# Kernel tuning notes

Measured on AMD Instinct MI355X. Metric: run time of the kernel, lower is better.

The kernel has to match this reference:

```python
import jax, jax.numpy as jnp
import numpy as np

IN_DIM, H1, H2, N_CLS, N_DOM = 7, 64, 128, 9, 2
N_S, E_S = 100000, 3200000
N_C, E_C = 512, 16384


def gcn_conv(x, edge_index, W, b):
    # PyG GCNConv: x' = D^{-1/2} (A + I) D^{-1/2} (x W) + b
    N = x.shape[0]
    h = x @ W
    loops = jnp.arange(N)
    row = jnp.concatenate([edge_index[0], loops])  # sources
    col = jnp.concatenate([edge_index[1], loops])  # targets
    deg = jax.ops.segment_sum(jnp.ones_like(col, dtype=h.dtype), col, num_segments=N)
    dis = jnp.where(deg > 0, jax.lax.rsqrt(deg), 0.0)
    norm = dis[row] * dis[col]
    out = jax.ops.segment_sum(h[row] * norm[:, None], col, num_segments=N)
    return out + b


def setup_inputs() -> dict:
    key = jax.random.key(0)
    ks = jax.random.split(key, 24)
    d = {}
    d['x_s'] = jax.random.normal(ks[0], (N_S, IN_DIM), dtype=jnp.float32)
    d['x_c'] = jax.random.normal(ks[1], (N_C, IN_DIM), dtype=jnp.float32)
    d['Q'] = jax.random.uniform(ks[2], (N_S, N_C), dtype=jnp.float32)
    d['edge_index_s'] = jax.random.randint(ks[3], (2, E_S), 0, N_S)
    d['edge_index_c'] = jax.random.randint(ks[4], (2, E_C), 0, N_C)
    s = 0.1
    d['W1s'] = jax.random.normal(ks[5], (IN_DIM, H1)) * s
    d['b1s'] = jnp.zeros((H1,), jnp.float32)
    d['W2s'] = jax.random.normal(ks[6], (H1, H2)) * s
    d['b2s'] = jnp.zeros((H2,), jnp.float32)
    d['W1c'] = jax.random.normal(ks[7], (IN_DIM, H1)) * s
    d['b1c'] = jnp.zeros((H1,), jnp.float32)
    d['W2c'] = jax.random.normal(ks[8], (H1, H2)) * s
    d['b2c'] = jnp.zeros((H2,), jnp.float32)
    d['A1'] = jax.random.normal(ks[9], (2 * H2, H2)) * s
    d['ab1'] = jnp.zeros((H2,), jnp.float32)
    d['A2'] = jax.random.normal(ks[10], (H2, 2)) * s
    d['ab2'] = jnp.zeros((2,), jnp.float32)
    d['Wcls'] = jax.random.normal(ks[11], (H2, N_CLS)) * s
    d['bcls'] = jnp.zeros((N_CLS,), jnp.float32)
    d['D1'] = jax.random.normal(ks[12], (H2, H1)) * s
    d['db1'] = jnp.zeros((H1,), jnp.float32)
    d['D2'] = jax.random.normal(ks[13], (H1, N_DOM)) * s
    d['db2'] = jnp.zeros((N_DOM,), jnp.float32)
    return d


def reference(x_s, x_c, Q, edge_index_s, edge_index_c,
              W1s, b1s, W2s, b2s, W1c, b1c, W2c, b2c,
              A1, ab1, A2, ab2, Wcls, bcls, D1, db1, D2, db2):
    # sample branch (eval mode: dropout is identity)
    xs = jax.nn.relu(gcn_conv(x_s, edge_index_s, W1s, b1s))
    xs = jax.nn.relu(gcn_conv(xs, edge_index_s, W2s, b2s))
    # cluster branch
    xc = jax.nn.relu(gcn_conv(x_c, edge_index_c, W1c, b1c))
    xc = jax.nn.relu(gcn_conv(xc, edge_index_c, W2c, b2c))
    # cross-graph decode
    xc_dec = Q @ xc  # [N_s, 128]
    fusion = jnp.concatenate([xs, xc_dec], axis=1)  # [N_s, 256]
    w = jax.nn.softmax(jax.nn.relu(fusion @ A1 + ab1) @ A2 + ab2, axis=1)
    fused = w[:, 0:1] * xs + w[:, 1:2] * xc_dec
    class_output = fused @ Wcls + bcls
    # gradient reversal is identity in forward
    domain_output = jax.nn.relu(fused @ D1 + db1) @ D2 + db2
    return (class_output, domain_output, fused)
```

## Files before the change

kernel.cpp:

```cpp
#include <hip/hip_runtime.h>
#include <cstdint>
#include <cstddef>

static constexpr int kNS = 100000;
static constexpr int kNC = 512;
static constexpr int kES = 3200000;
static constexpr int kEC = 16384;

static constexpr int kNB = (kNS + 63) / 64;
static constexpr int kNB8 = kNB * 8;
static constexpr int kCHUNK = 8192;
static constexpr int kNBLK = (kES + kCHUNK - 1) / kCHUNK;

static constexpr int kGemmQBlocks = (kNS + 63) / 64;
static constexpr int kAgg64Blocks = (kNS + 7) / 8;

typedef __attribute__((ext_vector_type(8))) short short8;
typedef __attribute__((ext_vector_type(4))) float f32x4;

__device__ __forceinline__ unsigned short f2bf(float f) {
  union { float f; unsigned u; } v; v.f = f;
  unsigned u = v.u;
  unsigned r = (u + 0x7fffu + ((u >> 16) & 1u)) >> 16;
  return (unsigned short)r;
}
__device__ __forceinline__ float bflo(unsigned v) { return __uint_as_float(v << 16); }
__device__ __forceinline__ float bfhi(unsigned v) { return __uint_as_float(v & 0xffff0000u); }
__device__ __forceinline__ float bf2f(unsigned short s) { return __uint_as_float(((unsigned)s) << 16); }

__global__ __launch_bounds__(256) void k_passA(const int* __restrict__ col, int E,
                                               int* __restrict__ counts) {
  __shared__ int hist[kNB];
  int t = threadIdx.x, bid = blockIdx.x;
  for (int j = t; j < kNB; j += 256) hist[j] = 0;
  __syncthreads();
  int base = bid * kCHUNK;
#pragma unroll 4
  for (int i = 0; i < kCHUNK / 256; i++) {
    int e = base + i * 256 + t;
    if (e < E) atomicAdd(&hist[col[e] >> 6], 1);
  }
  __syncthreads();
  int sub = bid & 7;
  for (int j = t; j < kNB; j += 256) {
    int v = hist[j];
    if (v) atomicAdd(&counts[j * 8 + sub], v);
  }
}

__global__ void k_scan_flat(const int* __restrict__ cnt, int n, int* __restrict__ starts,
                            int* __restrict__ cursor) {
  __shared__ int s[256];
  int t = threadIdx.x;
  int run = 0;
  for (int base = 0; base < n; base += 256) {
    int i = base + t;
    int v = (i < n) ? cnt[i] : 0;
    s[t] = v;
    __syncthreads();
    for (int o = 1; o < 256; o <<= 1) {
      int x = (t >= o) ? s[t - o] : 0;
      __syncthreads();
      s[t] += x;
      __syncthreads();
    }
    if (i < n) {
      int ex = run + s[t] - v;
      starts[i] = ex;
      cursor[i] = ex;
    }
    int tot = s[255];
    __syncthreads();
    run += tot;
  }
  if (t == 0) starts[n] = run;
}

__global__ __launch_bounds__(256) void k_passB(const int* __restrict__ row, const int* __restrict__ col,
                                               int E, int* __restrict__ cursor, unsigned* __restrict__ edg) {
  __shared__ int hist[kNB];
  int t = threadIdx.x, bid = blockIdx.x;
  int sub = bid & 7;
  for (int j = t; j < kNB; j += 256) hist[j] = 0;
  __syncthreads();
  int base = bid * kCHUNK;
#pragma unroll 4
  for (int i = 0; i < kCHUNK / 256; i++) {
    int e = base + i * 256 + t;
    if (e < E) atomicAdd(&hist[col[e] >> 6], 1);
  }
  __syncthreads();
  for (int j = t; j < kNB; j += 256) {
    int v = hist[j];
    hist[j] = v ? atomicAdd(&cursor[j * 8 + sub], v) : 0;
  }
  __syncthreads();
#pragma unroll 4
  for (int i = 0; i < kCHUNK / 256; i++) {
    int e = base + i * 256 + t;
    if (e < E) {
      int c = col[e];
      int pos = atomicAdd(&hist[c >> 6], 1);
      edg[pos] = ((unsigned)row[e] << 6) | (unsigned)(c & 63);
    }
  }
}

__global__ __launch_bounds__(256) void k_passC(const unsigned* __restrict__ edg,
                                               const int* __restrict__ bstarts,
                                               int* __restrict__ deg, int* __restrict__ nstarts,
                                               float* __restrict__ dis,
                                               int* __restrict__ srow, int N) {
  __shared__ int ldeg[64];
  __shared__ int lcur[64];
  int b = blockIdx.x, t = threadIdx.x;
  int s0 = bstarts[b * 8], s1 = bstarts[b * 8 + 8];
  if (t < 64) ldeg[t] = 0;
  __syncthreads();
  for (int i = s0 + t; i < s1; i += 256) atomicAdd(&ldeg[edg[i] & 63u], 1);
  __syncthreads();
  if (t < 64) {
    int own = ldeg[t];
    int incl = own;
#pragma unroll
    for (int off = 1; off < 64; off <<= 1) {
      int o = __shfl_up(incl, off);
      if (t >= off) incl += o;
    }
    int st = s0 + incl - own;
    lcur[t] = st;
    int g = b * 64 + t;
    if (g < N) {
      deg[g] = own;
      nstarts[g] = st;
      dis[g] = rsqrtf((float)(own + 1));
    }
  }
  __syncthreads();
  for (int i = s0 + t; i < s1; i += 256) {
    unsigned ew = edg[i];
    int pos = atomicAdd(&lcur[ew & 63u], 1);
    srow[pos] = (int)(ew >> 6);
  }
}

__global__ void k_hist(const int* __restrict__ col, int E, int* __restrict__ cnt) {
  int i = blockIdx.x * blockDim.x + threadIdx.x;
  if (i < E) atomicAdd(&cnt[col[i]], 1);
}

__global__ void k_dis(const int* __restrict__ cnt, int N, float* __restrict__ dis) {
  int i = blockIdx.x * blockDim.x + threadIdx.x;
  if (i < N) dis[i] = rsqrtf((float)(cnt[i] + 1));
}

__global__ void k_scan1(const int* __restrict__ cnt, int N, int* __restrict__ starts, int* __restrict__ bsum) {
  __shared__ int s[256];
  int t = threadIdx.x;
  int i = blockIdx.x * 256 + t;
  int v = (i < N) ? cnt[i] : 0;
  s[t] = v;
  __syncthreads();
  for (int o = 1; o < 256; o <<= 1) {
    int x = (t >= o) ? s[t - o] : 0;
    __syncthreads();
    s[t] += x;
    __syncthreads();
  }
  if (i < N) starts[i] = s[t] - v;
  if (t == 255) bsum[blockIdx.x] = s[255];
}

__global__ void k_scan2(int* __restrict__ bsum, int nb) {
  __shared__ int s[256];
  int t = threadIdx.x;
  int run = 0;
  for (int base = 0; base < nb; base += 256) {
    int i = base + t;
    int v = (i < nb) ? bsum[i] : 0;
    s[t] = v;
    __syncthreads();
    for (int o = 1; o < 256; o <<= 1) {
      int x = (t >= o) ? s[t - o] : 0;
      __syncthreads();
      s[t] += x;
      __syncthreads();
    }
    if (i < nb) bsum[i] = run + s[t] - v;
    int tot = s[255];
    __syncthreads();
    run += tot;
  }
}

__global__ void k_scan3(int* __restrict__ starts, int* __restrict__ cursor, const int* __restrict__ bsum, int N) {
  int i = blockIdx.x * 256 + threadIdx.x;
  if (i < N) {
    int v = starts[i] + bsum[blockIdx.x];
    starts[i] = v;
    cursor[i] = v;
  }
}

__global__ void k_scatter(const int* __restrict__ row, const int* __restrict__ col, int E,
                          int* __restrict__ cursor, int* __restrict__ srow) {
  int i = blockIdx.x * blockDim.x + threadIdx.x;
  if (i < E) {
    int pos = atomicAdd(&cursor[col[i]], 1);
    srow[pos] = row[i];
  }
}

__global__ __launch_bounds__(256) void k_z(const float* __restrict__ x, const float* __restrict__ dis,
                                           unsigned* __restrict__ z, int N) {
  int r = blockIdx.x * 256 + threadIdx.x;
  if (r >= N) return;
  const float* xr = x + (size_t)r * 7;
  float d = dis[r];
  unsigned w0 = (unsigned)f2bf(xr[0] * d) | ((unsigned)f2bf(xr[1] * d) << 16);
  unsigned w1 = (unsigned)f2bf(xr[2] * d) | ((unsigned)f2bf(xr[3] * d) << 16);
  unsigned w2 = (unsigned)f2bf(xr[4] * d) | ((unsigned)f2bf(xr[5] * d) << 16);
  unsigned w3 = (unsigned)f2bf(xr[6] * d);
  uint4 o = {w0, w1, w2, w3};
  *(uint4*)(z + (size_t)r * 4) = o;
}

__global__ __launch_bounds__(256) void k_agg7(const unsigned* __restrict__ z,
                                              const int* __restrict__ starts, const int* __restrict__ cnt,
                                              const int* __restrict__ srow, const float* __restrict__ dis,
                                              unsigned* __restrict__ a7, int N) {
  int c = blockIdx.x * 256 + threadIdx.x;
  if (c >= N) return;
  uint4 v = *(const uint4*)(z + (size_t)c * 4);
  float a0 = bflo(v.x), a1 = bfhi(v.x), a2 = bflo(v.y), a3 = bfhi(v.y);
  float a4 = bflo(v.z), a5 = bfhi(v.z), a6 = bflo(v.w), a7v = bfhi(v.w);
  int s0 = starts[c], n = cnt[c];
  const int* sp = srow + s0;
  int e = 0;
  for (; e + 4 <= n; e += 4) {
    uint4 w0 = *(const uint4*)(z + (size_t)sp[e] * 4);
    uint4 w1 = *(const uint4*)(z + (size_t)sp[e + 1] * 4);
    uint4 w2 = *(const uint4*)(z + (size_t)sp[e + 2] * 4);
    uint4 w3 = *(const uint4*)(z + (size_t)sp[e + 3] * 4);
    a0 += bflo(w0.x) + bflo(w1.x) + bflo(w2.x) + bflo(w3.x);
    a1 += bfhi(w0.x) + bfhi(w1.x) + bfhi(w2.x) + bfhi(w3.x);
    a2 += bflo(w0.y) + bflo(w1.y) + bflo(w2.y) + bflo(w3.y);
    a3 += bfhi(w0.y) + bfhi(w1.y) + bfhi(w2.y) + bfhi(w3.y);
    a4 += bflo(w0.z) + bflo(w1.z) + bflo(w2.z) + bflo(w3.z);
    a5 += bfhi(w0.z) + bfhi(w1.z) + bfhi(w2.z) + bfhi(w3.z);
    a6 += bflo(w0.w) + bflo(w1.w) + bflo(w2.w) + bflo(w3.w);
    a7v += bfhi(w0.w) + bfhi(w1.w) + bfhi(w2.w) + bfhi(w3.w);
  }
  for (; e < n; e++) {
    uint4 w = *(const uint4*)(z + (size_t)sp[e] * 4);
    a0 += bflo(w.x); a1 += bfhi(w.x); a2 += bflo(w.y); a3 += bfhi(w.y);
    a4 += bflo(w.z); a5 += bfhi(w.z); a6 += bflo(w.w); a7v += bfhi(w.w);
  }
  float d = dis[c];
  unsigned o0 = (unsigned)f2bf(a0 * d) | ((unsigned)f2bf(a1 * d) << 16);
  unsigned o1 = (unsigned)f2bf(a2 * d) | ((unsigned)f2bf(a3 * d) << 16);
  unsigned o2 = (unsigned)f2bf(a4 * d) | ((unsigned)f2bf(a5 * d) << 16);
  unsigned o3 = (unsigned)f2bf(a6 * d) | ((unsigned)f2bf(a7v * d) << 16);
  uint4 o = {o0, o1, o2, o3};
  *(uint4*)(a7 + (size_t)c * 4) = o;
}

__global__ __launch_bounds__(256) void k_lin7b(const unsigned* __restrict__ a7, const float* __restrict__ W,
                                               const float* __restrict__ b, const float* __restrict__ dis,
                                               unsigned short* __restrict__ y, int N) {
  __shared__ float Ws[7 * 64];
  int t = threadIdx.x;
  for (int j = t; j < 7 * 64; j += 256) Ws[j] = W[j];
  __syncthreads();
  int idx = blockIdx.x * 256 + t;
  if (idx < N * 32) {
    int r = idx >> 5, c2 = (idx & 31) * 2;
    uint4 v = *(const uint4*)(a7 + (size_t)r * 4);
    float a[7] = {bflo(v.x), bfhi(v.x), bflo(v.y), bfhi(v.y), bflo(v.z), bfhi(v.z), bflo(v.w)};
    float s0 = b[c2], s1 = b[c2 + 1];
#pragma unroll
    for (int k = 0; k < 7; k++) {
      s0 = fmaf(a[k], Ws[k * 64 + c2], s0);
      s1 = fmaf(a[k], Ws[k * 64 + c2 + 1], s1);
    }
    float d = dis[r];
    float y0 = fmaxf(s0, 0.f) * d;
    float y1 = fmaxf(s1, 0.f) * d;
    *(unsigned*)(y + (size_t)r * 64 + c2) = (unsigned)f2bf(y0) | ((unsigned)f2bf(y1) << 16);
  }
}

__device__ __forceinline__ void agg64_body(int bid, int t,
                                           const unsigned short* __restrict__ ys,
                                           const int* __restrict__ starts, const int* __restrict__ cnt,
                                           const int* __restrict__ srow, const float* __restrict__ dis,
                                           unsigned short* __restrict__ out, int N) {
  constexpr int F = 64, LPN = 32;
  int c = bid * (256 / LPN) + t / LPN;
  if (c >= N) return;
  int fi = (t % LPN) * 2;
  unsigned v = *(const unsigned*)(ys + (size_t)c * F + fi);
  float ax = bflo(v), ay = bfhi(v);
  int s0 = starts[c], n = cnt[c];
  const int* sp = srow + s0;
  int e = 0;
  for (; e + 8 <= n; e += 8) {
    int r0 = sp[e], r1 = sp[e + 1], r2 = sp[e + 2], r3 = sp[e + 3];
    int r4 = sp[e + 4], r5 = sp[e + 5], r6 = sp[e + 6], r7 = sp[e + 7];
    unsigned v0 = *(const unsigned*)(ys + (size_t)r0 * F + fi);
    unsigned v1 = *(const unsigned*)(ys + (size_t)r1 * F + fi);
    unsigned v2 = *(const unsigned*)(ys + (size_t)r2 * F + fi);
    unsigned v3 = *(const unsigned*)(ys + (size_t)r3 * F + fi);
    unsigned v4 = *(const unsigned*)(ys + (size_t)r4 * F + fi);
    unsigned v5 = *(const unsigned*)(ys + (size_t)r5 * F + fi);
    unsigned v6 = *(const unsigned*)(ys + (size_t)r6 * F + fi);
    unsigned v7 = *(const unsigned*)(ys + (size_t)r7 * F + fi);
    ax += bflo(v0) + bflo(v1) + bflo(v2) + bflo(v3) + bflo(v4) + bflo(v5) + bflo(v6) + bflo(v7);
    ay += bfhi(v0) + bfhi(v1) + bfhi(v2) + bfhi(v3) + bfhi(v4) + bfhi(v5) + bfhi(v6) + bfhi(v7);
  }
  for (; e + 4 <= n; e += 4) {
    int r0 = sp[e], r1 = sp[e + 1], r2 = sp[e + 2], r3 = sp[e + 3];
    unsigned v0 = *(const unsigned*)(ys + (size_t)r0 * F + fi);
    unsigned v1 = *(const unsigned*)(ys + (size_t)r1 * F + fi);
    unsigned v2 = *(const unsigned*)(ys + (size_t)r2 * F + fi);
    unsigned v3 = *(const unsigned*)(ys + (size_t)r3 * F + fi);
    ax += bflo(v0) + bflo(v1) + bflo(v2) + bflo(v3);
    ay += bfhi(v0) + bfhi(v1) + bfhi(v2) + bfhi(v3);
  }
  for (; e < n; e++) {
    unsigned vv = *(const unsigned*)(ys + (size_t)sp[e] * F + fi);
    ax += bflo(vv);
    ay += bfhi(vv);
  }
  float d = dis[c];
  *(unsigned*)(out + (size_t)c * F + fi) = (unsigned)f2bf(ax * d) | ((unsigned)f2bf(ay * d) << 16);
}

__global__ __launch_bounds__(256) void k_agg64(const unsigned short* __restrict__ ys,
                                               const int* __restrict__ starts, const int* __restrict__ cnt,
                                               const int* __restrict__ srow, const float* __restrict__ dis,
                                               unsigned short* __restrict__ out, int N) {
  agg64_body(blockIdx.x, threadIdx.x, ys, starts, cnt, srow, dis, out, N);
}

__global__ __launch_bounds__(256) void k_lin64x128(const unsigned short* __restrict__ xin, const float* __restrict__ W,
                                                   const float* __restrict__ b, unsigned short* __restrict__ hs, int N) {
  __shared__ float Ws[64 * 128];
  __shared__ float xs[32][64];
  int t = threadIdx.x;
  for (int j = t; j < 64 * 128; j += 256) Ws[j] = W[j];
  int r0 = blockIdx.x * 32;
  for (int j = t; j < 32 * 64; j += 256) {
    int r = j >> 6, k = j & 63;
    int gr = r0 + r;
    xs[r][k] = (gr < N) ? bf2f(xin[(size_t)gr * 64 + k]) : 0.f;
  }
  __syncthreads();
  int c = t & 63;
  int rb = (t >> 6) * 8;
  float a0[8], a1[8];
#pragma unroll
  for (int rr = 0; rr < 8; rr++) { a0[rr] = 0.f; a1[rr] = 0.f; }
  for (int k = 0; k < 64; k++) {
    float w0 = Ws[k * 128 + c];
    float w1 = Ws[k * 128 + c + 64];
#pragma unroll
    for (int rr = 0; rr < 8; rr++) {
      float xv = xs[rb + rr][k];
      a0[rr] = fmaf(xv, w0, a0[rr]);
      a1[rr] = fmaf(xv, w1, a1[rr]);
    }
  }
  float bb0 = b[c], bb1 = b[c + 64];
#pragma unroll
  for (int rr = 0; rr < 8; rr++) {
    int gr = r0 + rb + rr;
    if (gr < N) {
      hs[(size_t)gr * 128 + c] = f2bf(fmaxf(a0[rr] + bb0, 0.f));
      hs[(size_t)gr * 128 + c + 64] = f2bf(fmaxf(a1[rr] + bb1, 0.f));
    }
  }
}

__global__ void k_pack_all(const unsigned short* __restrict__ xc2b, const float* __restrict__ A1,
                           const float* __restrict__ D1, const float* __restrict__ Wcls,
                           short* __restrict__ Bq, short* __restrict__ A1p, short* __restrict__ Bh) {
  int i = blockIdx.x * 256 + threadIdx.x;
  if (i < 512 * 128) {
    int e = i;
    int k = e >> 7, n = e & 127;
    int frag = (k >> 5) * 8 + (n >> 4);
    int l = (n & 15) | (((k >> 3) & 3) << 4);
    int j = k & 7;
    Bq[(size_t)frag * 512 + l * 8 + j] = (short)xc2b[e];
  } else if (i < 512 * 128 + 256 * 128) {
    int e = i - 512 * 128;
    int k = e >> 7, n = e & 127;
    int frag = (k >> 5) * 8 + (n >> 4);
    int l = (n & 15) | (((k >> 3) & 3) << 4);
    int j = k & 7;
    A1p[(size_t)frag * 512 + l * 8 + j] = (short)f2bf(A1[e]);
  } else if (i < 512 * 128 + 256 * 128 + 128 * 80) {
    int e = i - (512 * 128 + 256 * 128);
    int k = e / 80, n = e % 80;
    float v = 0.f;
    if (n < 64) v = D1[k * 64 + n];
    else if (n < 73) v = Wcls[k * 9 + (n - 64)];
    int frag = (k >> 5) * 5 + (n >> 4);
    int l = (n & 15) | (((k >> 3) & 3) << 4);
    int j = k & 7;
    Bh[(size_t)frag * 512 + l * 8 + j] = (short)f2bf(v);
  }
}

__device__ __forceinline__ short8 zero8() {
  short8 z;
#pragma unroll
  for (int j = 0; j < 8; j++) z[j] = 0;
  return z;
}

__device__ __forceinline__ short8 cvt8(float4 v0, float4 v1) {
  short8 r;
  r[0] = (short)f2bf(v0.x); r[1] = (short)f2bf(v0.y); r[2] = (short)f2bf(v0.z); r[3] = (short)f2bf(v0.w);
  r[4] = (short)f2bf(v1.x); r[5] = (short)f2bf(v1.y); r[6] = (short)f2bf(v1.z); r[7] = (short)f2bf(v1.w);
  return r;
}

__device__ __forceinline__ short8 load_a_f32(const float* p, bool ok) {
  if (!ok) return zero8();
  return cvt8(*(const float4*)p, *(const float4*)(p + 4));
}

__device__ __forceinline__ void gemm_q_body(int bid, int t, const float* __restrict__ Q,
                                            const short* __restrict__ Bp,
                                            unsigned short* __restrict__ outb, int M) {
  int lane = t & 63;
  int wid = t >> 6;
  int m0 = bid * 64 + wid * 16;
  int mrow = lane & 15;
  int kg = lane >> 4;
  f32x4 acc[8];
#pragma unroll
  for (int nf = 0; nf < 8; nf++) acc[nf] = (f32x4){0.f, 0.f, 0.f, 0.f};
  int r0 = m0 + mrow;
  bool ok = r0 < M;
  const float* ap = Q + (size_t)r0 * 512 + kg * 8;
  const short* bl = Bp + lane * 8;
  float4 z4 = {0.f, 0.f, 0.f, 0.f};
  float4 v0 = ok ? *(const float4*)ap : z4;
  float4 v1 = ok ? *(const float4*)(ap + 4) : z4;
  for (int ks = 0; ks < 16; ks++) {
    float4 n0 = z4, n1 = z4;
    if (ks < 15 && ok) {
      n0 = *(const float4*)(ap + (ks + 1) * 32);
      n1 = *(const float4*)(ap + (ks + 1) * 32 + 4);
    }
    short8 a = cvt8(v0, v1);
    const short* bb = bl + (ks << 12);
#pragma unroll
    for (int nf = 0; nf < 8; nf++) {
      short8 b = *(const short8*)(bb + (nf << 9));
      acc[nf] = __builtin_amdgcn_mfma_f32_16x16x32_bf16(a, b, acc[nf], 0, 0, 0);
    }
    v0 = n0;
    v1 = n1;
  }
  int col = lane & 15;
  int g = lane >> 4;
#pragma unroll
  for (int nf = 0; nf < 8; nf++)
#pragma unroll
    for (int r = 0; r < 4; r++) {
      int row = m0 + g * 4 + r;
      if (row < M) outb[(size_t)row * 128 + nf * 16 + col] = f2bf(acc[nf][r]);
    }
}

__global__ __launch_bounds__(256) void k_aggq(const float* __restrict__ Q, const short* __restrict__ Bp,
                                              unsigned short* __restrict__ xcdb,
                                              const unsigned short* __restrict__ ys,
                                              const int* __restrict__ starts, const int* __restrict__ cnt,
                                              const int* __restrict__ srow, const float* __restrict__ dis,
                                              unsigned short* __restrict__ gt, int M) {
  int bid = blockIdx.x, t = threadIdx.x;
  if (bid < kGemmQBlocks) {
    gemm_q_body(bid, t, Q, Bp, xcdb, M);
  } else {
    agg64_body(bid - kGemmQBlocks, t, ys, starts, cnt, srow, dis, gt, M);
  }
}

__global__ __launch_bounds__(256) void k_gemm_fuse_mfma(const unsigned short* __restrict__ Xs,
                                                        const unsigned short* __restrict__ Xc,
                                                        const short* __restrict__ A1p, const float* __restrict__ ab1,
                                                        const float* __restrict__ A2, const float* __restrict__ ab2,
                                                        float* __restrict__ fused, int M) {
  int t = threadIdx.x;
  int lane = t & 63;
  int wid = t >> 6;
  int m0 = blockIdx.x * 64 + wid * 16;
  int mrow = lane & 15;
  int kg = lane >> 4;
  f32x4 acc[8];
#pragma unroll
  for (int nf = 0; nf < 8; nf++) acc[nf] = (f32x4){0.f, 0.f, 0.f, 0.f};
  int r0 = m0 + mrow;
  bool ok = r0 < M;
  const short* bl = A1p + lane * 8;
  short8 a = ok ? *(const short8*)(Xs + (size_t)r0 * 128 + kg * 8) : zero8();
  for (int ks = 0; ks < 8; ks++) {
    short8 an = zero8();
    if (ks < 7 && ok) {
      int ks1 = ks + 1;
      const unsigned short* src = (ks1 < 4) ? Xs : Xc;
      an = *(const short8*)(src + (size_t)r0 * 128 + (ks1 & 3) * 32 + kg * 8);
    }
    const short* bb = bl + (ks << 12);
#pragma unroll
    for (int nf = 0; nf < 8; nf++) {
      short8 b = *(const short8*)(bb + (nf << 9));
      acc[nf] = __builtin_amdgcn_mfma_f32_16x16x32_bf16(a, b, acc[nf], 0, 0, 0);
    }
    a = an;
  }
  int col16 = lane & 15;
  int g = lane >> 4;
  float bias[8], w20[8], w21[8];
#pragma unroll
  for (int nf = 0; nf < 8; nf++) {
    int cc = nf * 16 + col16;
    bias[nf] = ab1[cc];
    w20[nf] = A2[2 * cc];
    w21[nf] = A2[2 * cc + 1];
  }
  float b20 = ab2[0], b21 = ab2[1];
#pragma unroll
  for (int r = 0; r < 4; r++) {
    float u0 = 0.f, u1 = 0.f;
#pragma unroll
    for (int nf = 0; nf < 8; nf++) {
      float tv = fmaxf(acc[nf][r] + bias[nf], 0.f);
      u0 = fmaf(tv, w20[nf], u0);
      u1 = fmaf(tv, w21[nf], u1);
    }
#pragma unroll
    for (int off = 1; off < 16; off <<= 1) {
      u0 += __shfl_xor(u0, off);
      u1 += __shfl_xor(u1, off);
    }
    int row = m0 + g * 4 + r;
    if (row < M) {
      float ua = u0 + b20, ub = u1 + b21;
      float mx = fmaxf(ua, ub);
      float e0 = __expf(ua - mx), e1 = __expf(ub - mx);
      float inv = 1.f / (e0 + e1);
      float w0 = e0 * inv, w1 = e1 * inv;
      int p = col16;
      const unsigned short* xsp = Xs + (size_t)row * 128 + p * 8;
      const unsigned short* xcp = Xc + (size_t)row * 128 + p * 8;
      float* op = fused + (size_t)row * 128 + p * 8;
      float4 o0, o1;
      unsigned sx0 = *(const unsigned*)(xsp + 0), sx1 = *(const unsigned*)(xsp + 2);
      unsigned sx2 = *(const unsigned*)(xsp + 4), sx3 = *(const unsigned*)(xsp + 6);
      unsigned cx0 = *(const unsigned*)(xcp + 0), cx1 = *(const unsigned*)(xcp + 2);
      unsigned cx2 = *(const unsigned*)(xcp + 4), cx3 = *(const unsigned*)(xcp + 6);
      o0.x = w0 * bflo(sx0) + w1 * bflo(cx0);
      o0.y = w0 * bfhi(sx0) + w1 * bfhi(cx0);
      o0.z = w0 * bflo(sx1) + w1 * bflo(cx1);
      o0.w = w0 * bfhi(sx1) + w1 * bfhi(cx1);
      o1.x = w0 * bflo(sx2) + w1 * bflo(cx2);
      o1.y = w0 * bfhi(sx2) + w1 * bfhi(cx2);
      o1.z = w0 * bflo(sx3) + w1 * bflo(cx3);
      o1.w = w0 * bfhi(sx3) + w1 * bfhi(cx3);
      *(float4*)op = o0;
      *(float4*)(op + 4) = o1;
    }
  }
}

__global__ __launch_bounds__(256) void k_final_mfma(const float* __restrict__ fused, const short* __restrict__ Bh,
                                                    const float* __restrict__ bcls, const float* __restrict__ db1,
                                                    const float* __restrict__ D2, const float* __restrict__ db2,
                                                    float* __restrict__ cls_out, float* __restrict__ dom_out, int M) {
  int t = threadIdx.x;
  int lane = t & 63;
  int wid = t >> 6;
  int m0 = blockIdx.x * 128 + wid * 32;
  int mrow = lane & 15;
  int kg = lane >> 4;
  f32x4 acc[2][5];
#pragma unroll
  for (int mi = 0; mi < 2; mi++)
#pragma unroll
    for (int nf = 0; nf < 5; nf++) acc[mi][nf] = (f32x4){0.f, 0.f, 0.f, 0.f};
  int r0 = m0 + mrow, r1 = m0 + 16 + mrow;
  bool ok0 = r0 < M, ok1 = r1 < M;
  const float* a0p = fused + (size_t)r0 * 128 + kg * 8;
  const float* a1p = fused + (size_t)r1 * 128 + kg * 8;
  const short* bl = Bh + lane * 8;
  for (int ks = 0; ks < 4; ks++) {
    short8 a0 = load_a_f32(a0p + ks * 32, ok0);
    short8 a1 = load_a_f32(a1p + ks * 32, ok1);
    const short* bb = bl + ks * 5 * 512;
#pragma unroll
    for (int nf = 0; nf < 5; nf++) {
      short8 b = *(const short8*)(bb + (nf << 9));
      acc[0][nf] = __builtin_amdgcn_mfma_f32_16x16x32_bf16(a0, b, acc[0][nf], 0, 0, 0);
      acc[1][nf] = __builtin_amdgcn_mfma_f32_16x16x32_bf16(a1, b, acc[1][nf], 0, 0, 0);
    }
  }
  int col16 = lane & 15;
  int g = lane >> 4;
  float bh[4], d20[4], d21[4];
#pragma unroll
  for (int nf = 0; nf < 4; nf++) {
    int h = col16 + 16 * nf;
    bh[nf] = db1[h];
    d20[nf] = D2[h * 2];
    d21[nf] = D2[h * 2 + 1];
  }
  float bc = (col16 < 9) ? bcls[col16] : 0.f;
  float b20 = db2[0], b21 = db2[1];
#pragma unroll
  for (int mi = 0; mi < 2; mi++) {
#pragma unroll
    for (int r = 0; r < 4; r++) {
      float p0 = 0.f, p1 = 0.f;
#pragma unroll
      for (int nf = 0; nf < 4; nf++) {
        float hv = fmaxf(acc[mi][nf][r] + bh[nf], 0.f);
        p0 = fmaf(hv, d20[nf], p0);
        p1 = fmaf(hv, d21[nf], p1);
      }
#pragma unroll
      for (int off = 1; off < 16; off <<= 1) {
        p0 += __shfl_xor(p0, off);
        p1 += __shfl_xor(p1, off);
      }
      int row = m0 + mi * 16 + g * 4 + r;
      if (row < M) {
        if (col16 < 9) cls_out[(size_t)row * 9 + col16] = acc[mi][4][r] + bc;
        if (col16 == 0) {
          dom_out[(size_t)row * 2 + 0] = p0 + b20;
          dom_out[(size_t)row * 2 + 1] = p1 + b21;
        }
      }
    }
  }
}

extern "C" void kernel_launch(void* const* d_in, const int* in_sizes, int n_in,
                              void* d_out, int out_size, void* d_ws, size_t ws_size,
                              hipStream_t stream) {
  const float* x_s = (const float*)d_in[0];
  const float* x_c = (const float*)d_in[1];
  const float* Q = (const float*)d_in[2];
  const int* eis = (const int*)d_in[3];
  const int* eic = (const int*)d_in[4];
  const float* W1s = (const float*)d_in[5];
  const float* b1s = (const float*)d_in[6];
  const float* W2s = (const float*)d_in[7];
  const float* b2s = (const float*)d_in[8];
  const float* W1c = (const float*)d_in[9];
  const float* b1c = (const float*)d_in[10];
  const float* W2c = (const float*)d_in[11];
  const float* b2c = (const float*)d_in[12];
  const float* A1 = (const float*)d_in[13];
  const float* ab1 = (const float*)d_in[14];
  const float* A2 = (const float*)d_in[15];
  const float* ab2 = (const float*)d_in[16];
  const float* Wcls = (const float*)d_in[17];
  const float* bcls = (const float*)d_in[18];
  const float* D1 = (const float*)d_in[19];
  const float* db1 = (const float*)d_in[20];
  const float* D2 = (const float*)d_in[21];
  const float* db2 = (const float*)d_in[22];

  float* out_cls = (float*)d_out;
  float* out_dom = out_cls + (size_t)kNS * 9;
  float* out_fus = out_dom + (size_t)kNS * 2;

  char* p = (char*)d_ws;
  auto alloc = [&](size_t bytes) -> void* {
    void* r = (void*)p;
    p += (bytes + 255) & ~(size_t)255;
    return r;
  };
  int* deg_s = (int*)alloc((size_t)kNS * 4);
  float* dis_s = (float*)alloc((size_t)kNS * 4);
  int* nstarts_s = (int*)alloc((size_t)kNS * 4);
  int* counts_s = (int*)alloc((size_t)kNB8 * 4);
  int* bstarts_s = (int*)alloc((size_t)(kNB8 + 1) * 4);
  int* bcursor_s = (int*)alloc((size_t)kNB8 * 4);
  int* srow_s = (int*)alloc((size_t)kES * 4);
  unsigned* edg_s = (unsigned*)alloc((size_t)kES * 4);
  int* deg_c = (int*)alloc((size_t)kNC * 4);
  int* cstarts_c = (int*)alloc((size_t)kNC * 4);
  int* cursor_c = (int*)alloc((size_t)kNC * 4);
  int* bsum_c = (int*)alloc(512 * 4);
  float* dis_c = (float*)alloc((size_t)kNC * 4);
  int* srow_c = (int*)alloc((size_t)kEC * 4);
  unsigned* zs = (unsigned*)alloc((size_t)kNS * 16);
  unsigned* a7s = (unsigned*)alloc((size_t)kNS * 16);
  unsigned short* ys = (unsigned short*)alloc((size_t)kNS * 64 * 2);
  unsigned short* gts = (unsigned short*)alloc((size_t)kNS * 64 * 2);
  unsigned short* xs2b = (unsigned short*)alloc((size_t)kNS * 128 * 2);
  unsigned short* xcdb = (unsigned short*)alloc((size_t)kNS * 128 * 2);
  unsigned* zc = (unsigned*)alloc((size_t)kNC * 16);
  unsigned* a7c = (unsigned*)alloc((size_t)kNC * 16);
  unsigned short* yc = (unsigned short*)alloc((size_t)kNC * 64 * 2);
  unsigned short* gtc = (unsigned short*)alloc((size_t)kNC * 64 * 2);
  unsigned short* xc2b = (unsigned short*)alloc((size_t)kNC * 128 * 2);
  short* Bq = (short*)alloc((size_t)512 * 128 * 2);
  short* A1p = (short*)alloc((size_t)256 * 128 * 2);
  short* Bh = (short*)alloc((size_t)128 * 80 * 2);
  (void)ws_size; (void)in_sizes; (void)n_in; (void)out_size;

  hipMemsetAsync(counts_s, 0, (size_t)kNB8 * 4, stream);
  hipMemsetAsync(deg_c, 0, (size_t)kNC * 4, stream);

  const int nbC = (kNC + 255) / 256;
  const int nbS = (kNS + 255) / 256;

  k_passA<<<kNBLK, 256, 0, stream>>>(eis + kES, kES, counts_s);
  k_scan_flat<<<1, 256, 0, stream>>>(counts_s, kNB8, bstarts_s, bcursor_s);
  k_passB<<<kNBLK, 256, 0, stream>>>(eis, eis + kES, kES, bcursor_s, edg_s);
  k_passC<<<kNB, 256, 0, stream>>>(edg_s, bstarts_s, deg_s, nstarts_s, dis_s, srow_s, kNS);

  k_hist<<<(kEC + 255) / 256, 256, 0, stream>>>(eic + kEC, kEC, deg_c);
  k_dis<<<nbC, 256, 0, stream>>>(deg_c, kNC, dis_c);
  k_scan1<<<nbC, 256, 0, stream>>>(deg_c, kNC, cstarts_c, bsum_c);
  k_scan2<<<1, 256, 0, stream>>>(bsum_c, nbC);
  k_scan3<<<nbC, 256, 0, stream>>>(cstarts_c, cursor_c, bsum_c, kNC);
  k_scatter<<<(kEC + 255) / 256, 256, 0, stream>>>(eic, eic + kEC, kEC, cursor_c, srow_c);

  k_z<<<(kNC + 255) / 256, 256, 0, stream>>>(x_c, dis_c, zc, kNC);
  k_agg7<<<(kNC + 255) / 256, 256, 0, stream>>>(zc, cstarts_c, deg_c, srow_c, dis_c, a7c, kNC);
  k_lin7b<<<(kNC * 32 + 255) / 256, 256, 0, stream>>>(a7c, W1c, b1c, dis_c, yc, kNC);
  k_agg64<<<(kNC + 7) / 8, 256, 0, stream>>>(yc, cstarts_c, deg_c, srow_c, dis_c, gtc, kNC);
  k_lin64x128<<<(kNC + 31) / 32, 256, 0, stream>>>(gtc, W2c, b2c, xc2b, kNC);
  k_pack_all<<<(512 * 128 + 256 * 128 + 128 * 80 + 255) / 256, 256, 0, stream>>>(xc2b, A1, D1, Wcls, Bq, A1p, Bh);

  k_z<<<nbS, 256, 0, stream>>>(x_s, dis_s, zs, kNS);
  k_agg7<<<nbS, 256, 0, stream>>>(zs, nstarts_s, deg_s, srow_s, dis_s, a7s, kNS);
  k_lin7b<<<(kNS * 32 + 255) / 256, 256, 0, stream>>>(a7s, W1s, b1s, dis_s, ys, kNS);

  k_aggq<<<kGemmQBlocks + kAgg64Blocks, 256, 0, stream>>>(Q, Bq, xcdb,
                                                          ys, nstarts_s, deg_s, srow_s, dis_s, gts, kNS);

  k_lin64x128<<<(kNS + 31) / 32, 256, 0, stream>>>(gts, W2s, b2s, xs2b, kNS);

  k_gemm_fuse_mfma<<<(kNS + 63) / 64, 256, 0, stream>>>(xs2b, xcdb, A1p, ab1, A2, ab2, out_fus, kNS);
  k_final_mfma<<<(kNS + 127) / 128, 256, 0, stream>>>(out_fus, Bh, bcls, db1, D2, db2, out_cls, out_dom, kNS);
}
```

Baseline: 488.9 us.

## Split Q-GEMM across fused kernels to overlap with CSR build passes

The Q@xc GEMM blocks are divided into three groups and co-launched with the sample-graph CSR build passes (passB, passC) and the 64-wide aggregation. This lets the compute-heavy GEMM overlap the atomic- and memory-bound sort passes. It also folds k_z into passC, and replaces the cluster graph's three-kernel scan plus k_dis with a single-block flat scan that also writes dis. Mixing different kinds of work in one launch can leave blocks unevenly balanced, and the cluster pack must now finish before the CSR passes can start.

```diff
diff --git a/kernel.cpp b/kernel.cpp
--- a/kernel.cpp
+++ b/kernel.cpp
@@ -14,6 +14,9 @@
 
 static constexpr int kGemmQBlocks = (kNS + 63) / 64;
 static constexpr int kAgg64Blocks = (kNS + 7) / 8;
+static constexpr int kG1 = 625;
+static constexpr int kG2 = 469;
+static constexpr int kG3 = kGemmQBlocks - kG1 - kG2;
 
 typedef __attribute__((ext_vector_type(8))) short short8;
 typedef __attribute__((ext_vector_type(4))) float f32x4;
@@ -49,7 +52,7 @@
 }
 
 __global__ void k_scan_flat(const int* __restrict__ cnt, int n, int* __restrict__ starts,
-                            int* __restrict__ cursor) {
+                            int* __restrict__ cursor, float* __restrict__ dis) {
   __shared__ int s[256];
   int t = threadIdx.x;
   int run = 0;
@@ -68,6 +71,7 @@
       int ex = run + s[t] - v;
       starts[i] = ex;
       cursor[i] = ex;
+      if (dis) dis[i] = rsqrtf((float)(v + 1));
     }
     int tot = s[255];
     __syncthreads();
@@ -76,10 +80,10 @@
   if (t == 0) starts[n] = run;
 }
 
-__global__ __launch_bounds__(256) void k_passB(const int* __restrict__ row, const int* __restrict__ col,
-                                               int E, int* __restrict__ cursor, unsigned* __restrict__ edg) {
+__device__ __forceinline__ void passB_body(int bid, int t, const int* __restrict__ row,
+                                           const int* __restrict__ col, int E,
+                                           int* __restrict__ cursor, unsigned* __restrict__ edg) {
   __shared__ int hist[kNB];
-  int t = threadIdx.x, bid = blockIdx.x;
   int sub = bid & 7;
   for (int j = t; j < kNB; j += 256) hist[j] = 0;
   __syncthreads();
@@ -106,14 +110,13 @@
   }
 }
 
-__global__ __launch_bounds__(256) void k_passC(const unsigned* __restrict__ edg,
-                                               const int* __restrict__ bstarts,
-                                               int* __restrict__ deg, int* __restrict__ nstarts,
-                                               float* __restrict__ dis,
-                                               int* __restrict__ srow, int N) {
+__device__ __forceinline__ void passC_body(int b, int t, const unsigned* __restrict__ edg,
+                                           const int* __restrict__ bstarts,
+                                           int* __restrict__ deg, int* __restrict__ nstarts,
+                                           float* __restrict__ dis, int* __restrict__ srow,
+                                           const float* __restrict__ x, unsigned* __restrict__ z, int N) {
   __shared__ int ldeg[64];
   __shared__ int lcur[64];
-  int b = blockIdx.x, t = threadIdx.x;
   int s0 = bstarts[b * 8], s1 = bstarts[b * 8 + 8];
   if (t < 64) ldeg[t] = 0;
   __syncthreads();
@@ -133,7 +136,15 @@
     if (g < N) {
       deg[g] = own;
       nstarts[g] = st;
-      dis[g] = rsqrtf((float)(own + 1));
+      float d = rsqrtf((float)(own + 1));
+      dis[g] = d;
+      const float* xr = x + (size_t)g * 7;
+      unsigned w0 = (unsigned)f2bf(xr[0] * d) | ((unsigned)f2bf(xr[1] * d) << 16);
+      unsigned w1 = (unsigned)f2bf(xr[2] * d) | ((unsigned)f2bf(xr[3] * d) << 16);
+      unsigned w2 = (unsigned)f2bf(xr[4] * d) | ((unsigned)f2bf(xr[5] * d) << 16);
+      unsigned w3 = (unsigned)f2bf(xr[6] * d);
+      uint4 o = {w0, w1, w2, w3};
+      *(uint4*)(z + (size_t)g * 4) = o;
     }
   }
   __syncthreads();
@@ -147,59 +158,6 @@
 __global__ void k_hist(const int* __restrict__ col, int E, int* __restrict__ cnt) {
   int i = blockIdx.x * blockDim.x + threadIdx.x;
   if (i < E) atomicAdd(&cnt[col[i]], 1);
-}
-
-__global__ void k_dis(const int* __restrict__ cnt, int N, float* __restrict__ dis) {
-  int i = blockIdx.x * blockDim.x + threadIdx.x;
-  if (i < N) dis[i] = rsqrtf((float)(cnt[i] + 1));
-}
-
-__global__ void k_scan1(const int* __restrict__ cnt, int N, int* __restrict__ starts, int* __restrict__ bsum) {
-  __shared__ int s[256];
-  int t = threadIdx.x;
-  int i = blockIdx.x * 256 + t;
-  int v = (i < N) ? cnt[i] : 0;
-  s[t] = v;
-  __syncthreads();
-  for (int o = 1; o < 256; o <<= 1) {
-    int x = (t >= o) ? s[t - o] : 0;
-    __syncthreads();
-    s[t] += x;
-    __syncthreads();
-  }
-  if (i < N) starts[i] = s[t] - v;
-  if (t == 255) bsum[blockIdx.x] = s[255];
-}
-
-__global__ void k_scan2(int* __restrict__ bsum, int nb) {
-  __shared__ int s[256];
-  int t = threadIdx.x;
-  int run = 0;
-  for (int base = 0; base < nb; base += 256) {
-    int i = base + t;
-    int v = (i < nb) ? bsum[i] : 0;
-    s[t] = v;
-    __syncthreads();
-    for (int o = 1; o < 256; o <<= 1) {
-      int x = (t >= o) ? s[t - o] : 0;
-      __syncthreads();
-      s[t] += x;
-      __syncthreads();
-    }
-    if (i < nb) bsum[i] = run + s[t] - v;
-    int tot = s[255];
-    __syncthreads();
-    run += tot;
-  }
-}
-
-__global__ void k_scan3(int* __restrict__ starts, int* __restrict__ cursor, const int* __restrict__ bsum, int N) {
-  int i = blockIdx.x * 256 + threadIdx.x;
-  if (i < N) {
-    int v = starts[i] + bsum[blockIdx.x];
-    starts[i] = v;
-    cursor[i] = v;
-  }
 }
 
 __global__ void k_scatter(const int* __restrict__ row, const int* __restrict__ col, int E,
@@ -477,18 +435,35 @@
     }
 }
 
-__global__ __launch_bounds__(256) void k_aggq(const float* __restrict__ Q, const short* __restrict__ Bp,
+__global__ __launch_bounds__(256) void k_fatB(const float* __restrict__ Q, const short* __restrict__ Bq,
+                                              unsigned short* __restrict__ xcdb, int M,
+                                              const int* __restrict__ row, const int* __restrict__ col, int E,
+                                              int* __restrict__ cursor, unsigned* __restrict__ edg) {
+  int bid = blockIdx.x, t = threadIdx.x;
+  if (bid < kG1) gemm_q_body(bid, t, Q, Bq, xcdb, M);
+  else passB_body(bid - kG1, t, row, col, E, cursor, edg);
+}
+
+__global__ __launch_bounds__(256) void k_fatC(const float* __restrict__ Q, const short* __restrict__ Bq,
+                                              unsigned short* __restrict__ xcdb, int M,
+                                              const unsigned* __restrict__ edg, const int* __restrict__ bstarts,
+                                              int* __restrict__ deg, int* __restrict__ nstarts,
+                                              float* __restrict__ dis, int* __restrict__ srow,
+                                              const float* __restrict__ xs, unsigned* __restrict__ zs) {
+  int bid = blockIdx.x, t = threadIdx.x;
+  if (bid < kG2) gemm_q_body(kG1 + bid, t, Q, Bq, xcdb, M);
+  else passC_body(bid - kG2, t, edg, bstarts, deg, nstarts, dis, srow, xs, zs, M);
+}
+
+__global__ __launch_bounds__(256) void k_fatA(const float* __restrict__ Q, const short* __restrict__ Bq,
                                               unsigned short* __restrict__ xcdb,
                                               const unsigned short* __restrict__ ys,
                                               const int* __restrict__ starts, const int* __restrict__ cnt,
                                               const int* __restrict__ srow, const float* __restrict__ dis,
                                               unsigned short* __restrict__ gt, int M) {
   int bid = blockIdx.x, t = threadIdx.x;
-  if (bid < kGemmQBlocks) {
-    gemm_q_body(bid, t, Q, Bp, xcdb, M);
-  } else {
-    agg64_body(bid - kGemmQBlocks, t, ys, starts, cnt, srow, dis, gt, M);
-  }
+  if (bid < kG3) gemm_q_body(kG1 + kG2 + bid, t, Q, Bq, xcdb, M);
+  else agg64_body(bid - kG3, t, ys, starts, cnt, srow, dis, gt, M);
 }
 
 __global__ __launch_bounds__(256) void k_gemm_fuse_mfma(const unsigned short* __restrict__ Xs,
@@ -696,9 +671,8 @@
   int* srow_s = (int*)alloc((size_t)kES * 4);
   unsigned* edg_s = (unsigned*)alloc((size_t)kES * 4);
   int* deg_c = (int*)alloc((size_t)kNC * 4);
-  int* cstarts_c = (int*)alloc((size_t)kNC * 4);
+  int* cstarts_c = (int*)alloc((size_t)(kNC + 1) * 4);
   int* cursor_c = (int*)alloc((size_t)kNC * 4);
-  int* bsum_c = (int*)alloc(512 * 4);
   float* dis_c = (float*)alloc((size_t)kNC * 4);
   int* srow_c = (int*)alloc((size_t)kEC * 4);
   unsigned* zs = (unsigned*)alloc((size_t)kNS * 16);
@@ -720,21 +694,12 @@
   hipMemsetAsync(counts_s, 0, (size_t)kNB8 * 4, stream);
   hipMemsetAsync(deg_c, 0, (size_t)kNC * 4, stream);
 
-  const int nbC = (kNC + 255) / 256;
-  const int nbS = (kNS + 255) / 256;
-
   k_passA<<<kNBLK, 256, 0, stream>>>(eis + kES, kES, counts_s);
-  k_scan_flat<<<1, 256, 0, stream>>>(counts_s, kNB8, bstarts_s, bcursor_s);
-  k_passB<<<kNBLK, 256, 0, stream>>>(eis, eis + kES, kES, bcursor_s, edg_s);
-  k_passC<<<kNB, 256, 0, stream>>>(edg_s, bstarts_s, deg_s, nstarts_s, dis_s, srow_s, kNS);
+  k_scan_flat<<<1, 256, 0, stream>>>(counts_s, kNB8, bstarts_s, bcursor_s, nullptr);
 
   k_hist<<<(kEC + 255) / 256, 256, 0, stream>>>(eic + kEC, kEC, deg_c);
-  k_dis<<<nbC, 256, 0, stream>>>(deg_c, kNC, dis_c);
-  k_scan1<<<nbC, 256, 0, stream>>>(deg_c, kNC, cstarts_c, bsum_c);
-  k_scan2<<<1, 256, 0, stream>>>(bsum_c, nbC);
-  k_scan3<<<nbC, 256, 0, stream>>>(cstarts_c, cursor_c, bsum_c, kNC);
+  k_scan_flat<<<1, 256, 0, stream>>>(deg_c, kNC, cstarts_c, cursor_c, dis_c);
   k_scatter<<<(kEC + 255) / 256, 256, 0, stream>>>(eic, eic + kEC, kEC, cursor_c, srow_c);
-
   k_z<<<(kNC + 255) / 256, 256, 0, stream>>>(x_c, dis_c, zc, kNC);
   k_agg7<<<(kNC + 255) / 256, 256, 0, stream>>>(zc, cstarts_c, deg_c, srow_c, dis_c, a7c, kNC);
   k_lin7b<<<(kNC * 32 + 255) / 256, 256, 0, stream>>>(a7c, W1c, b1c, dis_c, yc, kNC);
@@ -742,12 +707,13 @@
   k_lin64x128<<<(kNC + 31) / 32, 256, 0, stream>>>(gtc, W2c, b2c, xc2b, kNC);
   k_pack_all<<<(512 * 128 + 256 * 128 + 128 * 80 + 255) / 256, 256, 0, stream>>>(xc2b, A1, D1, Wcls, Bq, A1p, Bh);
 
-  k_z<<<nbS, 256, 0, stream>>>(x_s, dis_s, zs, kNS);
-  k_agg7<<<nbS, 256, 0, stream>>>(zs, nstarts_s, deg_s, srow_s, dis_s, a7s, kNS);
+  k_fatB<<<kG1 + kNBLK, 256, 0, stream>>>(Q, Bq, xcdb, kNS, eis, eis + kES, kES, bcursor_s, edg_s);
+  k_fatC<<<kG2 + kNB, 256, 0, stream>>>(Q, Bq, xcdb, kNS, edg_s, bstarts_s, deg_s, nstarts_s, dis_s, srow_s, x_s, zs);
+
+  k_agg7<<<(kNS + 255) / 256, 256, 0, stream>>>(zs, nstarts_s, deg_s, srow_s, dis_s, a7s, kNS);
   k_lin7b<<<(kNS * 32 + 255) / 256, 256, 0, stream>>>(a7s, W1s, b1s, dis_s, ys, kNS);
 
-  k_aggq<<<kGemmQBlocks + kAgg64Blocks, 256, 0, stream>>>(Q, Bq, xcdb,
-                                                          ys, nstarts_s, deg_s, srow_s, dis_s, gts, kNS);
+  k_fatA<<<kG3 + kAgg64Blocks, 256, 0, stream>>>(Q, Bq, xcdb, ys, nstarts_s, deg_s, srow_s, dis_s, gts, kNS);
 
   k_lin64x128<<<(kNS + 31) / 32, 256, 0, stream>>>(gts, W2s, b2s, xs2b, kNS);
 
```

New measurement: 480.2 us. Within noise of the previous version (-1.8%).
